# Optimization experiments

Measured on AMD Instinct MI355X. Metric: run time of the kernel, lower is better.

Reference implementation:

```python
import jax, jax.numpy as jnp
import numpy as np

N_NODES = 100000
N_EDGES = 1600000
IN_DIM = 128
HID_DIM = 64
OUT_DIM = 128
EPS = 1e-5


def setup_inputs() -> dict:
    key = jax.random.key(0)
    ks = jax.random.split(key, 10)
    feat = jax.random.normal(ks[0], (N_NODES, IN_DIM), dtype=jnp.float32)
    src = jax.random.randint(ks[1], (N_EDGES,), 0, N_NODES)
    dst = jax.random.randint(ks[2], (N_EDGES,), 0, N_NODES)
    # learned params
    gamma = jnp.ones((IN_DIM,), jnp.float32)
    beta = jnp.zeros((IN_DIM,), jnp.float32)
    Wq = jax.random.normal(ks[3], (IN_DIM, HID_DIM), jnp.float32) * 0.05
    bq = jax.random.normal(ks[4], (HID_DIM,), jnp.float32) * 0.05
    Wk = jax.random.normal(ks[5], (IN_DIM, HID_DIM), jnp.float32) * 0.05
    Wv = jax.random.normal(ks[6], (IN_DIM, OUT_DIM), jnp.float32) * 0.05
    We = jax.random.normal(ks[7], (HID_DIM, 1), jnp.float32) * 0.05
    return {"feat": feat, "src": src, "dst": dst, "gamma": gamma, "beta": beta,
            "Wq": Wq, "bq": bq, "Wk": Wk, "Wv": Wv, "We": We}


def reference(feat, src, dst, gamma, beta, Wq, bq, Wk, Wv, We):
    # BatchNorm1d (training-mode batch stats, biased variance)
    mean = jnp.mean(feat, axis=0)
    var = jnp.mean((feat - mean) ** 2, axis=0)
    x = (feat - mean) * jax.lax.rsqrt(var + EPS) * gamma + beta
    # feat_drop = 0.0 -> identity
    q = x @ Wq + bq          # [N, H]
    k = x @ Wk               # [N, H]
    v = x @ Wv               # [N, O]
    # u_add_v: src-node q + dst-node k per edge, then sigmoid and fc_e -> scalar score
    e = jax.nn.sigmoid(q[src] + k[dst]) @ We  # [E, 1]
    e = e[:, 0]                               # [E]
    # edge_softmax: softmax over incoming edges of each destination node
    m = jax.ops.segment_max(e, dst, num_segments=N_NODES)  # [N]
    ex = jnp.exp(e - m[dst])
    s = jax.ops.segment_sum(ex, dst, num_segments=N_NODES)  # [N]
    a = ex / s[dst]                                          # [E]
    # u_mul_e_sum: weighted scatter-sum of source v into destinations
    rst = jax.ops.segment_sum(v[src] * a[:, None], dst, num_segments=N_NODES)  # [N, O]
    return rst
```

## Files before the change

kernel.cpp:

```cpp
#include <hip/hip_runtime.h>
#include <math.h>

#define IN_DIM 128
#define HID 64
#define OUT_DIM 128
#define ELL_W 64
constexpr float EPS = 1e-5f;

typedef short short8 __attribute__((ext_vector_type(8)));
typedef float f32x4  __attribute__((ext_vector_type(4)));


__device__ inline ushort f2bf(float x) {
    __bf16 h = (__bf16)x;
    return *reinterpret_cast<ushort*>(&h);
}
__device__ inline short f2bfs(float x) {
    __bf16 h = (__bf16)x;
    return *reinterpret_cast<short*>(&h);
}
__device__ inline float bf2f(ushort u) {
    union { unsigned u; float f; } c; c.u = ((unsigned)u) << 16;
    return c.f;
}
__device__ inline float4 bf4_to_f4(ushort4 u) {
    return make_float4(bf2f(u.x), bf2f(u.y), bf2f(u.z), bf2f(u.w));
}

__global__ __launch_bounds__(256) void stats_kernel(
    const float* __restrict__ feat, float* __restrict__ ws, int n_nodes)
{
    int col  = threadIdx.x & 127;
    int half = threadIdx.x >> 7;
    float sum = 0.f, sq = 0.f;
    for (int r = blockIdx.x * 2 + half; r < n_nodes; r += gridDim.x * 2) {
        float x = feat[r * IN_DIM + col];
        sum += x; sq += x * x;
    }
    __shared__ float redS[256], redQ[256];
    redS[threadIdx.x] = sum; redQ[threadIdx.x] = sq;
    __syncthreads();
    if (threadIdx.x < 128) {
        sum = redS[threadIdx.x] + redS[threadIdx.x + 128];
        sq  = redQ[threadIdx.x] + redQ[threadIdx.x + 128];
        unsafeAtomicAdd(&ws[col], sum);
        unsafeAtomicAdd(&ws[128 + col], sq);
    }
}

__global__ __launch_bounds__(256) void wprep(
    const float* __restrict__ Wq, const float* __restrict__ Wk,
    const float* __restrict__ Wv, ushort* __restrict__ Bfrag)
{
    int gid  = blockIdx.x * 256 + threadIdx.x;
    int f    = gid >> 6;
    int lane = gid & 63;
    int kc = f & 3, ct = (f >> 2) & 3, w = f >> 4;
    int col   = w * 64 + ct * 16 + (lane & 15);
    int kbase = kc * 32 + (lane >> 4) * 8;
    ushort tmp[8];
    #pragma unroll
    for (int j = 0; j < 8; j++) {
        int k = kbase + j;
        float val;
        if (col < 64)       val = Wq[k * HID + col];
        else if (col < 128) val = Wk[k * HID + (col - 64)];
        else                val = Wv[k * OUT_DIM + (col - 128)];
        tmp[j] = f2bf(val);
    }
    ushort* d = &Bfrag[(f * 64 + lane) * 8];
    *(ushort4*)d       = make_ushort4(tmp[0], tmp[1], tmp[2], tmp[3]);
    *(ushort4*)(d + 4) = make_ushort4(tmp[4], tmp[5], tmp[6], tmp[7]);
}

__global__ __launch_bounds__(256) void mfma_qkv(
    const float* __restrict__ feat, const ushort* __restrict__ Bfrag,
    const float* __restrict__ bq,
    const float* __restrict__ gamma, const float* __restrict__ beta,
    const float* __restrict__ stats,
    ushort* __restrict__ qb, ushort* __restrict__ kb, ushort* __restrict__ vb,
    int n_nodes)
{
    __shared__ float sc[IN_DIM], sh[IN_DIM];
    int tid = threadIdx.x;
    if (tid < 128) {
        float inv_n = 1.0f / (float)n_nodes;
        float mean = stats[tid] * inv_n;
        float var  = stats[128 + tid] * inv_n - mean * mean;
        float s    = gamma[tid] * rsqrtf(var + EPS);
        sc[tid] = s; sh[tid] = beta[tid] - mean * s;
    }

    int w    = tid >> 6;
    int lane = tid & 63;
    int row0 = blockIdx.x * 64;
    int m    = lane & 15;
    int quad = lane >> 4;
    int nm1  = n_nodes - 1;

    short8 bfr[16];
    #pragma unroll
    for (int f = 0; f < 16; f++)
        bfr[f] = *(const short8*)&Bfrag[((w * 16 + f) * 64 + lane) * 8];

    __syncthreads();

    f32x4 acc[4][4] = {};

    #pragma unroll
    for (int kc = 0; kc < 4; kc++) {
        int koff = kc * 32 + quad * 8;
        float4 sc0 = *(const float4*)&sc[koff];
        float4 sc1 = *(const float4*)&sc[koff + 4];
        float4 sh0 = *(const float4*)&sh[koff];
        float4 sh1 = *(const float4*)&sh[koff + 4];
        short8 afr[4];
        #pragma unroll
        for (int rt = 0; rt < 4; rt++) {
            int row = row0 + rt * 16 + m;
            row = row < nm1 ? row : nm1;
            const float* fp = &feat[(size_t)row * IN_DIM + koff];
            float4 x0 = *(const float4*)fp;
            float4 x1 = *(const float4*)(fp + 4);
            afr[rt][0] = f2bfs(x0.x * sc0.x + sh0.x);
            afr[rt][1] = f2bfs(x0.y * sc0.y + sh0.y);
            afr[rt][2] = f2bfs(x0.z * sc0.z + sh0.z);
            afr[rt][3] = f2bfs(x0.w * sc0.w + sh0.w);
            afr[rt][4] = f2bfs(x1.x * sc1.x + sh1.x);
            afr[rt][5] = f2bfs(x1.y * sc1.y + sh1.y);
            afr[rt][6] = f2bfs(x1.z * sc1.z + sh1.z);
            afr[rt][7] = f2bfs(x1.w * sc1.w + sh1.w);
        }
        #pragma unroll
        for (int rt = 0; rt < 4; rt++)
            #pragma unroll
            for (int ct = 0; ct < 4; ct++)
                acc[rt][ct] = __builtin_amdgcn_mfma_f32_16x16x32_bf16(
                    afr[rt], bfr[ct * 4 + kc], acc[rt][ct], 0, 0, 0);
    }

    ushort* base; int ld, cl;
    if (w == 0)      { base = qb; ld = HID;     cl = 0; }
    else if (w == 1) { base = kb; ld = HID;     cl = 0; }
    else             { base = vb; ld = OUT_DIM; cl = (w - 2) * 64; }

    #pragma unroll
    for (int ct = 0; ct < 4; ct++) {
        int col = cl + ct * 16 + m;
        float bias = (w == 0) ? bq[ct * 16 + m] : 0.f;
        #pragma unroll
        for (int rt = 0; rt < 4; rt++) {
            int r0 = row0 + rt * 16 + quad * 4;
            #pragma unroll
            for (int r = 0; r < 4; r++)
                base[(size_t)(r0 + r) * ld + col] = f2bf(acc[rt][ct][r] + bias);
        }
    }
}

__global__ __launch_bounds__(256) void fill_ell(
    const int* __restrict__ src, const int* __restrict__ dst,
    int* __restrict__ deg, int* __restrict__ ell, int n_edges)
{
    int stride = gridDim.x * 256;
    for (int e = blockIdx.x * 256 + threadIdx.x; e < n_edges; e += stride) {
        int d = dst[e];
        int s = src[e];
        int pos = atomicAdd(&deg[d], 1);
        if (pos < ELL_W) ell[d * ELL_W + pos] = s;
    }
}

__global__ __launch_bounds__(256) void hist_kernel(
    const int* __restrict__ dst, int* __restrict__ deg, int n_edges)
{
    int e = blockIdx.x * 256 + threadIdx.x;
    if (e < n_edges) atomicAdd(&deg[dst[e]], 1);
}

#define SCAN_B 256

__global__ __launch_bounds__(256) void scan_partial(
    const int* __restrict__ deg, int* __restrict__ part, int n)
{
    int chunk = (n + SCAN_B - 1) / SCAN_B;
    int lo = blockIdx.x * chunk;
    int hi = lo + chunk; if (hi > n) hi = n;
    int s = 0;
    for (int i = lo + threadIdx.x; i < hi; i += 256) s += deg[i];
    __shared__ int red[256];
    red[threadIdx.x] = s; __syncthreads();
    for (int d = 128; d; d >>= 1) {
        if (threadIdx.x < d) red[threadIdx.x] += red[threadIdx.x + d];
        __syncthreads();
    }
    if (threadIdx.x == 0) part[blockIdx.x] = red[0];
}

__global__ __launch_bounds__(256) void scan_combine(
    int* __restrict__ part, int* __restrict__ offsets, int n)
{
    __shared__ int tmp[256];
    int t = threadIdx.x;
    int v = part[t];
    tmp[t] = v; __syncthreads();
    for (int d = 1; d < 256; d <<= 1) {
        int cur = tmp[t];
        int add = (t >= d) ? tmp[t - d] : 0;
        __syncthreads();
        tmp[t] = cur + add;
        __syncthreads();
    }
    part[t] = tmp[t] - v;
    if (t == 255) offsets[n] = tmp[255];
}

__global__ __launch_bounds__(256) void scan_final(
    const int* __restrict__ deg, const int* __restrict__ part,
    int* __restrict__ offsets, int* __restrict__ cursor, int n)
{
    __shared__ int tmp[256];
    int t = threadIdx.x;
    int chunk = (n + SCAN_B - 1) / SCAN_B;
    int lo = blockIdx.x * chunk;
    int hi = lo + chunk; if (hi > n) hi = n;
    int base = part[blockIdx.x];
    for (int i0 = lo; i0 < hi; i0 += 256) {
        int i = i0 + t;
        int d = (i < hi) ? deg[i] : 0;
        tmp[t] = d; __syncthreads();
        for (int s = 1; s < 256; s <<= 1) {
            int cur = tmp[t];
            int add = (t >= s) ? tmp[t - s] : 0;
            __syncthreads();
            tmp[t] = cur + add;
            __syncthreads();
        }
        int excl = tmp[t] - d;
        int total = tmp[255];
        if (i < hi) { offsets[i] = base + excl; cursor[i] = base + excl; }
        base += total;
        __syncthreads();
    }
}

__global__ __launch_bounds__(256) void fill_kernel(
    const int* __restrict__ src, const int* __restrict__ dst,
    int* __restrict__ cursor, int* __restrict__ csr_src, int n_edges)
{
    int e = blockIdx.x * 256 + threadIdx.x;
    if (e < n_edges) {
        int d = dst[e];
        int pos = atomicAdd(&cursor[d], 1);
        csr_src[pos] = src[e];
    }
}

__device__ inline void gather_core(
    const int* __restrict__ row, int cnt, int node, int h, int sub,
    const ushort* __restrict__ qb, const ushort* __restrict__ kb,
    const ushort* __restrict__ vb, const float* __restrict__ We,
    float* __restrict__ out)
{
    if (cnt == 0) {
        if (sub == 0) {
            float4 z = make_float4(0.f, 0.f, 0.f, 0.f);
            *(float4*)&out[node * OUT_DIM + 4 * h]      = z;
            *(float4*)&out[node * OUT_DIM + 64 + 4 * h] = z;
        }
        return;
    }

    float4 kd = bf4_to_f4(*(const ushort4*)&kb[node * HID + 4 * h]);
    float4 we = *(const float4*)&We[4 * h];

    float4 o0 = make_float4(0.f, 0.f, 0.f, 0.f);
    float4 o1 = make_float4(0.f, 0.f, 0.f, 0.f);
    float ssum = 0.f;

    for (int p0 = 0; p0 < cnt; p0 += 4) {
        int p = p0 + sub;
        bool act = (p < cnt);
        int sN = row[act ? p : 0];
        float4 qv = bf4_to_f4(*(const ushort4*)&qb[sN * HID + 4 * h]);
        float t;
        t  = we.x * __fdividef(1.f, 1.f + __expf(-(qv.x + kd.x)));
        t += we.y * __fdividef(1.f, 1.f + __expf(-(qv.y + kd.y)));
        t += we.z * __fdividef(1.f, 1.f + __expf(-(qv.z + kd.z)));
        t += we.w * __fdividef(1.f, 1.f + __expf(-(qv.w + kd.w)));
        t += __shfl_xor(t, 1);
        t += __shfl_xor(t, 2);
        t += __shfl_xor(t, 4);
        t += __shfl_xor(t, 8);
        float exv = act ? __expf(t) : 0.f;
        ssum += exv;
        float4 v0 = bf4_to_f4(*(const ushort4*)&vb[sN * OUT_DIM + 4 * h]);
        float4 v1 = bf4_to_f4(*(const ushort4*)&vb[sN * OUT_DIM + 64 + 4 * h]);
        o0.x += exv * v0.x; o0.y += exv * v0.y;
        o0.z += exv * v0.z; o0.w += exv * v0.w;
        o1.x += exv * v1.x; o1.y += exv * v1.y;
        o1.z += exv * v1.z; o1.w += exv * v1.w;
    }

    ssum += __shfl_xor(ssum, 16); ssum += __shfl_xor(ssum, 32);
    o0.x += __shfl_xor(o0.x, 16); o0.x += __shfl_xor(o0.x, 32);
    o0.y += __shfl_xor(o0.y, 16); o0.y += __shfl_xor(o0.y, 32);
    o0.z += __shfl_xor(o0.z, 16); o0.z += __shfl_xor(o0.z, 32);
    o0.w += __shfl_xor(o0.w, 16); o0.w += __shfl_xor(o0.w, 32);
    o1.x += __shfl_xor(o1.x, 16); o1.x += __shfl_xor(o1.x, 32);
    o1.y += __shfl_xor(o1.y, 16); o1.y += __shfl_xor(o1.y, 32);
    o1.z += __shfl_xor(o1.z, 16); o1.z += __shfl_xor(o1.z, 32);
    o1.w += __shfl_xor(o1.w, 16); o1.w += __shfl_xor(o1.w, 32);

    if (sub == 0) {
        float inv = (ssum > 0.f) ? __fdividef(1.f, ssum) : 0.f;
        o0.x *= inv; o0.y *= inv; o0.z *= inv; o0.w *= inv;
        o1.x *= inv; o1.y *= inv; o1.z *= inv; o1.w *= inv;
        *(float4*)&out[node * OUT_DIM + 4 * h]      = o0;
        *(float4*)&out[node * OUT_DIM + 64 + 4 * h] = o1;
    }
}

__global__ __launch_bounds__(256) void gather_ell(
    const int* __restrict__ deg, const int* __restrict__ ell,
    const ushort* __restrict__ qb, const ushort* __restrict__ kb,
    const ushort* __restrict__ vb, const float* __restrict__ We,
    float* __restrict__ out, int n_nodes)
{
    int node = (blockIdx.x * 256 + threadIdx.x) >> 6;
    int lane = threadIdx.x & 63;
    if (node >= n_nodes) return;
    int cnt = deg[node];
    cnt = cnt < ELL_W ? cnt : ELL_W;
    gather_core(&ell[(size_t)node * ELL_W], cnt, node,
                lane & 15, lane >> 4, qb, kb, vb, We, out);
}

__global__ __launch_bounds__(256) void gather_csr(
    const int* __restrict__ offsets, const int* __restrict__ csr_src,
    const ushort* __restrict__ qb, const ushort* __restrict__ kb,
    const ushort* __restrict__ vb, const float* __restrict__ We,
    float* __restrict__ out, int n_nodes)
{
    int node = (blockIdx.x * 256 + threadIdx.x) >> 6;
    int lane = threadIdx.x & 63;
    if (node >= n_nodes) return;
    int beg = offsets[node];
    int cnt = offsets[node + 1] - beg;
    gather_core(&csr_src[beg], cnt, node,
                lane & 15, lane >> 4, qb, kb, vb, We, out);
}

extern "C" void kernel_launch(void* const* d_in, const int* in_sizes, int n_in,
                              void* d_out, int out_size, void* d_ws, size_t ws_size,
                              hipStream_t stream)
{
    const float* feat  = (const float*)d_in[0];
    const int*   src   = (const int*)d_in[1];
    const int*   dst   = (const int*)d_in[2];
    const float* gamma = (const float*)d_in[3];
    const float* beta  = (const float*)d_in[4];
    const float* Wq    = (const float*)d_in[5];
    const float* bq    = (const float*)d_in[6];
    const float* Wk    = (const float*)d_in[7];
    const float* Wv    = (const float*)d_in[8];
    const float* We    = (const float*)d_in[9];

    int n_nodes = in_sizes[0] / IN_DIM;
    int n_edges = in_sizes[1];
    int n_pad   = n_nodes + 64;
    size_t bfelems = (size_t)n_pad * (HID + HID + OUT_DIM) + 64 * 64 * 8;

    float* ws = (float*)d_ws;

    size_t ell_floats = 256 + (size_t)n_nodes * (1 + ELL_W) + 4;
    size_t ell_need   = (ell_floats + (bfelems + 1) / 2) * 4;

    int eb = (n_edges + 255) / 256;

    if (ws_size >= ell_need) {
        int* deg = (int*)(ws + 256);
        int* ell = deg + n_nodes;
        size_t off = 256 + (size_t)n_nodes * (1 + ELL_W);
        off = (off + 3) & ~(size_t)3;
        ushort* qb    = (ushort*)(ws + off);
        ushort* kb    = qb + (size_t)n_pad * HID;
        ushort* vb    = kb + (size_t)n_pad * HID;
        ushort* Bfrag = vb + (size_t)n_pad * OUT_DIM;

        hipMemsetAsync(ws, 0, (256 + (size_t)n_nodes) * sizeof(float), stream);
        stats_kernel<<<256, 256, 0, stream>>>(feat, ws, n_nodes);
        wprep<<<16, 256, 0, stream>>>(Wq, Wk, Wv, Bfrag);
        fill_ell<<<(n_edges + 1023) / 1024, 256, 0, stream>>>(
            src, dst, deg, ell, n_edges);
        mfma_qkv<<<(n_nodes + 63) / 64, 256, 0, stream>>>(
            feat, Bfrag, bq, gamma, beta, ws, qb, kb, vb, n_nodes);
        long long g_threads = (long long)n_nodes * 64;
        gather_ell<<<(int)((g_threads + 255) / 256), 256, 0, stream>>>(
            deg, ell, qb, kb, vb, We, (float*)d_out, n_nodes);
    } else {
        int* deg     = (int*)(ws + 256);
        int* offsets = deg + n_nodes;
        int* cursor  = offsets + n_nodes + 1;
        int* part    = cursor + n_nodes;
        int* csr_src = part + SCAN_B;
        size_t off = 256 + 3 * (size_t)n_nodes + 1 + SCAN_B + (size_t)n_edges;
        off = (off + 3) & ~(size_t)3;
        ushort* qb    = (ushort*)(ws + off);
        ushort* kb    = qb + (size_t)n_pad * HID;
        ushort* vb    = kb + (size_t)n_pad * HID;
        ushort* Bfrag = vb + (size_t)n_pad * OUT_DIM;

        hipMemsetAsync(ws, 0, (256 + (size_t)n_nodes) * sizeof(float), stream);
        stats_kernel<<<256, 256, 0, stream>>>(feat, ws, n_nodes);
        wprep<<<16, 256, 0, stream>>>(Wq, Wk, Wv, Bfrag);
        hist_kernel<<<eb, 256, 0, stream>>>(dst, deg, n_edges);
        scan_partial<<<SCAN_B, 256, 0, stream>>>(deg, part, n_nodes);
        scan_combine<<<1, 256, 0, stream>>>(part, offsets, n_nodes);
        scan_final<<<SCAN_B, 256, 0, stream>>>(deg, part, offsets, cursor, n_nodes);
        fill_kernel<<<eb, 256, 0, stream>>>(src, dst, cursor, csr_src, n_edges);
        mfma_qkv<<<(n_nodes + 63) / 64, 256, 0, stream>>>(
            feat, Bfrag, bq, gamma, beta, ws, qb, kb, vb, n_nodes);
        long long g_threads = (long long)n_nodes * 64;
        gather_csr<<<(int)((g_threads + 255) / 256), 256, 0, stream>>>(
            offsets, csr_src, qb, kb, vb, We, (float*)d_out, n_nodes);
    }
}
```

Baseline: 421.1 us.

## Partition ELL fill by destination range across block groups with vector loads

Replaces the single-pass ELL fill with a partitioned version. Blocks are split into 8 groups, and each group handles only edges whose destination falls in its node range. The aim is to localize atomics and ELL scatter writes (which blocks, and so which L2/XCD caches, touch which nodes). Edge arrays are now read as 4-wide nontemporal vector loads. The cost is that every group re-reads the full src/dst arrays, so index traffic grows by about 8x.

```diff
diff --git a/kernel.cpp b/kernel.cpp
--- a/kernel.cpp
+++ b/kernel.cpp
@@ -5,10 +5,12 @@
 #define HID 64
 #define OUT_DIM 128
 #define ELL_W 64
+#define NPART 8
 constexpr float EPS = 1e-5f;
 
 typedef short short8 __attribute__((ext_vector_type(8)));
 typedef float f32x4  __attribute__((ext_vector_type(4)));
+typedef int   i32x4  __attribute__((ext_vector_type(4)));
 
 
 __device__ inline ushort f2bf(float x) {
@@ -158,16 +160,42 @@
     }
 }
 
-__global__ __launch_bounds__(256) void fill_ell(
+__global__ __launch_bounds__(256) void fill_ell_part(
     const int* __restrict__ src, const int* __restrict__ dst,
-    int* __restrict__ deg, int* __restrict__ ell, int n_edges)
-{
-    int stride = gridDim.x * 256;
-    for (int e = blockIdx.x * 256 + threadIdx.x; e < n_edges; e += stride) {
-        int d = dst[e];
-        int s = src[e];
-        int pos = atomicAdd(&deg[d], 1);
-        if (pos < ELL_W) ell[d * ELL_W + pos] = s;
+    int* __restrict__ deg, int* __restrict__ ell,
+    int n_edges, int part_size)
+{
+    int p  = blockIdx.x & (NPART - 1);
+    int gb = blockIdx.x >> 3;
+    int nb = gridDim.x >> 3;
+    unsigned lo = (unsigned)(p * part_size);
+    unsigned ps = (unsigned)part_size;
+
+    int idx    = gb * 256 + threadIdx.x;
+    int stride = nb * 256;
+    int n4     = n_edges >> 2;
+
+    const i32x4* dst4 = reinterpret_cast<const i32x4*>(dst);
+    const i32x4* src4 = reinterpret_cast<const i32x4*>(src);
+
+    for (int i = idx; i < n4; i += stride) {
+        i32x4 d4 = __builtin_nontemporal_load(dst4 + i);
+        i32x4 s4 = __builtin_nontemporal_load(src4 + i);
+        #pragma unroll
+        for (int j = 0; j < 4; j++) {
+            unsigned d = (unsigned)d4[j];
+            if (d - lo < ps) {
+                int pos = atomicAdd(&deg[d], 1);
+                if (pos < ELL_W) ell[(size_t)d * ELL_W + pos] = s4[j];
+            }
+        }
+    }
+    for (int e = (n4 << 2) + idx; e < n_edges; e += stride) {
+        unsigned d = (unsigned)dst[e];
+        if (d - lo < ps) {
+            int pos = atomicAdd(&deg[d], 1);
+            if (pos < ELL_W) ell[(size_t)d * ELL_W + pos] = src[e];
+        }
     }
 }
 
@@ -388,11 +416,13 @@
         ushort* vb    = kb + (size_t)n_pad * HID;
         ushort* Bfrag = vb + (size_t)n_pad * OUT_DIM;
 
+        int part_size = (n_nodes + NPART - 1) / NPART;
+
         hipMemsetAsync(ws, 0, (256 + (size_t)n_nodes) * sizeof(float), stream);
         stats_kernel<<<256, 256, 0, stream>>>(feat, ws, n_nodes);
         wprep<<<16, 256, 0, stream>>>(Wq, Wk, Wv, Bfrag);
-        fill_ell<<<(n_edges + 1023) / 1024, 256, 0, stream>>>(
-            src, dst, deg, ell, n_edges);
+        fill_ell_part<<<2048, 256, 0, stream>>>(
+            src, dst, deg, ell, n_edges, part_size);
         mfma_qkv<<<(n_nodes + 63) / 64, 256, 0, stream>>>(
             feat, Bfrag, bq, gamma, beta, ws, qb, kb, vb, n_nodes);
         long long g_threads = (long long)n_nodes * 64;
```

After: 408.8 us. -2.9%, faster.

## Replace global-atomic ELL build with binned counting sort and LDS-local ELL gather

Applied to the files above, without the earlier changes.

Drops the global atomic ELL/CSR construction. Edges are now binned by 64-node destination block through per-workgroup LDS histograms, a scan, and an LDS-atomic scatter into a packed (local dst, src) array. The gather kernel rebuilds each block's ELL in shared memory before computing. Q and V are interleaved into one 192-wide row so each source node's values are fetched together. The goal is to cut global atomic contention and the large ELL memory traffic. The cost is more kernel launches and only 64 workgroups for the hist and scatter passes, which limits parallelism. Neighbour order within a node becomes nondeterministic, and any node with more than 64 in-edges is still truncated.

```diff
diff --git a/kernel.cpp b/kernel.cpp
--- a/kernel.cpp
+++ b/kernel.cpp
@@ -5,6 +5,8 @@
 #define HID 64
 #define OUT_DIM 128
 #define ELL_W 64
+#define NWG 64
+#define SCAN_B 256
 constexpr float EPS = 1e-5f;
 
 typedef short short8 __attribute__((ext_vector_type(8)));
@@ -78,7 +80,7 @@
     const float* __restrict__ bq,
     const float* __restrict__ gamma, const float* __restrict__ beta,
     const float* __restrict__ stats,
-    ushort* __restrict__ qb, ushort* __restrict__ kb, ushort* __restrict__ vb,
+    ushort* __restrict__ qvb, ushort* __restrict__ kb,
     int n_nodes)
 {
     __shared__ float sc[IN_DIM], sh[IN_DIM];
@@ -140,9 +142,8 @@
     }
 
     ushort* base; int ld, cl;
-    if (w == 0)      { base = qb; ld = HID;     cl = 0; }
-    else if (w == 1) { base = kb; ld = HID;     cl = 0; }
-    else             { base = vb; ld = OUT_DIM; cl = (w - 2) * 64; }
+    if (w == 1)      { base = kb;  ld = HID; cl = 0; }
+    else             { base = qvb; ld = 192; cl = (w == 0) ? 0 : 64 * (w - 1); }
 
     #pragma unroll
     for (int ct = 0; ct < 4; ct++) {
@@ -158,27 +159,22 @@
     }
 }
 
-__global__ __launch_bounds__(256) void fill_ell(
-    const int* __restrict__ src, const int* __restrict__ dst,
-    int* __restrict__ deg, int* __restrict__ ell, int n_edges)
-{
-    int stride = gridDim.x * 256;
-    for (int e = blockIdx.x * 256 + threadIdx.x; e < n_edges; e += stride) {
-        int d = dst[e];
-        int s = src[e];
-        int pos = atomicAdd(&deg[d], 1);
-        if (pos < ELL_W) ell[d * ELL_W + pos] = s;
-    }
-}
-
-__global__ __launch_bounds__(256) void hist_kernel(
-    const int* __restrict__ dst, int* __restrict__ deg, int n_edges)
-{
-    int e = blockIdx.x * 256 + threadIdx.x;
-    if (e < n_edges) atomicAdd(&deg[dst[e]], 1);
-}
-
-#define SCAN_B 256
+__global__ __launch_bounds__(256) void hist_bins(
+    const int* __restrict__ dst, int* __restrict__ histT,
+    int n_edges, int nbk, int chunk)
+{
+    extern __shared__ int cnt[];
+    int w = blockIdx.x, t = threadIdx.x;
+    for (int b = t; b < nbk; b += 256) cnt[b] = 0;
+    __syncthreads();
+    int lo = w * chunk;
+    int hi = lo + chunk; if (hi > n_edges) hi = n_edges;
+    for (int e = lo + t; e < hi; e += 256)
+        atomicAdd(&cnt[dst[e] >> 6], 1);
+    __syncthreads();
+    for (int b = t; b < nbk; b += 256)
+        histT[b * NWG + w] = cnt[b];
+}
 
 __global__ __launch_bounds__(256) void scan_partial(
     const int* __restrict__ deg, int* __restrict__ part, int n)
@@ -244,23 +240,29 @@
     }
 }
 
-__global__ __launch_bounds__(256) void fill_kernel(
+__global__ __launch_bounds__(256) void scatter_bins(
     const int* __restrict__ src, const int* __restrict__ dst,
-    int* __restrict__ cursor, int* __restrict__ csr_src, int n_edges)
-{
-    int e = blockIdx.x * 256 + threadIdx.x;
-    if (e < n_edges) {
+    const int* __restrict__ offs, int* __restrict__ packed,
+    int n_edges, int nbk, int chunk)
+{
+    extern __shared__ int cur[];
+    int w = blockIdx.x, t = threadIdx.x;
+    for (int b = t; b < nbk; b += 256) cur[b] = offs[b * NWG + w];
+    __syncthreads();
+    int lo = w * chunk;
+    int hi = lo + chunk; if (hi > n_edges) hi = n_edges;
+    for (int e = lo + t; e < hi; e += 256) {
         int d = dst[e];
-        int pos = atomicAdd(&cursor[d], 1);
-        csr_src[pos] = src[e];
-    }
-}
-
-__device__ inline void gather_core(
-    const int* __restrict__ row, int cnt, int node, int h, int sub,
-    const ushort* __restrict__ qb, const ushort* __restrict__ kb,
-    const ushort* __restrict__ vb, const float* __restrict__ We,
-    float* __restrict__ out)
+        int b = d >> 6;
+        int pos = atomicAdd(&cur[b], 1);
+        packed[pos] = (int)(((unsigned)(d & 63) << 26) | (unsigned)src[e]);
+    }
+}
+
+__device__ __forceinline__ void gather_core(
+    const int* row, int cnt, int node, int h, int sub,
+    const ushort* __restrict__ qvb, const ushort* __restrict__ kb,
+    const float* __restrict__ We, float* __restrict__ out)
 {
     if (cnt == 0) {
         if (sub == 0) {
@@ -282,20 +284,21 @@
         int p = p0 + sub;
         bool act = (p < cnt);
         int sN = row[act ? p : 0];
-        float4 qv = bf4_to_f4(*(const ushort4*)&qb[sN * HID + 4 * h]);
+        const ushort* qv = qvb + (size_t)sN * 192;
+        float4 qq = bf4_to_f4(*(const ushort4*)(qv + 4 * h));
         float t;
-        t  = we.x * __fdividef(1.f, 1.f + __expf(-(qv.x + kd.x)));
-        t += we.y * __fdividef(1.f, 1.f + __expf(-(qv.y + kd.y)));
-        t += we.z * __fdividef(1.f, 1.f + __expf(-(qv.z + kd.z)));
-        t += we.w * __fdividef(1.f, 1.f + __expf(-(qv.w + kd.w)));
+        t  = we.x * __fdividef(1.f, 1.f + __expf(-(qq.x + kd.x)));
+        t += we.y * __fdividef(1.f, 1.f + __expf(-(qq.y + kd.y)));
+        t += we.z * __fdividef(1.f, 1.f + __expf(-(qq.z + kd.z)));
+        t += we.w * __fdividef(1.f, 1.f + __expf(-(qq.w + kd.w)));
         t += __shfl_xor(t, 1);
         t += __shfl_xor(t, 2);
         t += __shfl_xor(t, 4);
         t += __shfl_xor(t, 8);
         float exv = act ? __expf(t) : 0.f;
         ssum += exv;
-        float4 v0 = bf4_to_f4(*(const ushort4*)&vb[sN * OUT_DIM + 4 * h]);
-        float4 v1 = bf4_to_f4(*(const ushort4*)&vb[sN * OUT_DIM + 64 + 4 * h]);
+        float4 v0 = bf4_to_f4(*(const ushort4*)(qv + 64 + 4 * h));
+        float4 v1 = bf4_to_f4(*(const ushort4*)(qv + 128 + 4 * h));
         o0.x += exv * v0.x; o0.y += exv * v0.y;
         o0.z += exv * v0.z; o0.w += exv * v0.w;
         o1.x += exv * v1.x; o1.y += exv * v1.y;
@@ -321,34 +324,42 @@
     }
 }
 
-__global__ __launch_bounds__(256) void gather_ell(
-    const int* __restrict__ deg, const int* __restrict__ ell,
-    const ushort* __restrict__ qb, const ushort* __restrict__ kb,
-    const ushort* __restrict__ vb, const float* __restrict__ We,
+__global__ __launch_bounds__(256) void gather_fused(
+    const int* __restrict__ offs, const int* __restrict__ packed,
+    const ushort* __restrict__ qvb, const ushort* __restrict__ kb,
+    const float* __restrict__ We,
     float* __restrict__ out, int n_nodes)
 {
-    int node = (blockIdx.x * 256 + threadIdx.x) >> 6;
-    int lane = threadIdx.x & 63;
-    if (node >= n_nodes) return;
-    int cnt = deg[node];
-    cnt = cnt < ELL_W ? cnt : ELL_W;
-    gather_core(&ell[(size_t)node * ELL_W], cnt, node,
-                lane & 15, lane >> 4, qb, kb, vb, We, out);
-}
-
-__global__ __launch_bounds__(256) void gather_csr(
-    const int* __restrict__ offsets, const int* __restrict__ csr_src,
-    const ushort* __restrict__ qb, const ushort* __restrict__ kb,
-    const ushort* __restrict__ vb, const float* __restrict__ We,
-    float* __restrict__ out, int n_nodes)
-{
-    int node = (blockIdx.x * 256 + threadIdx.x) >> 6;
-    int lane = threadIdx.x & 63;
-    if (node >= n_nodes) return;
-    int beg = offsets[node];
-    int cnt = offsets[node + 1] - beg;
-    gather_core(&csr_src[beg], cnt, node,
-                lane & 15, lane >> 4, qb, kb, vb, We, out);
+    __shared__ int deg_l[64];
+    __shared__ int ell_l[64][ELL_W];
+    int b = blockIdx.x;
+    int t = threadIdx.x;
+    if (t < 64) deg_l[t] = 0;
+    __syncthreads();
+
+    int beg = offs[b * NWG];
+    int end = offs[(b + 1) * NWG];
+    for (int e = beg + t; e < end; e += 256) {
+        int p = packed[e];
+        int dl = (int)((unsigned)p >> 26);
+        int pos = atomicAdd(&deg_l[dl], 1);
+        if (pos < ELL_W) ell_l[dl][pos] = p & 0x03FFFFFF;
+    }
+    __syncthreads();
+
+    int wv   = t >> 6;
+    int lane = t & 63;
+    int h    = lane & 15;
+    int sub  = lane >> 4;
+    #pragma unroll 1
+    for (int i = 0; i < 16; i++) {
+        int dl = wv * 16 + i;
+        int node = (b << 6) + dl;
+        if (node >= n_nodes) break;
+        int cnt = deg_l[dl];
+        cnt = cnt < ELL_W ? cnt : ELL_W;
+        gather_core(&ell_l[dl][0], cnt, node, h, sub, qvb, kb, We, out);
+    }
 }
 
 extern "C" void kernel_launch(void* const* d_in, const int* in_sizes, int n_in,
@@ -369,60 +380,37 @@
     int n_nodes = in_sizes[0] / IN_DIM;
     int n_edges = in_sizes[1];
     int n_pad   = n_nodes + 64;
-    size_t bfelems = (size_t)n_pad * (HID + HID + OUT_DIM) + 64 * 64 * 8;
+    int nbk     = (n_nodes + 63) >> 6;
+    int nidx    = nbk * NWG;
+    int chunk   = (n_edges + NWG - 1) / NWG;
 
     float* ws = (float*)d_ws;
 
-    size_t ell_floats = 256 + (size_t)n_nodes * (1 + ELL_W) + 4;
-    size_t ell_need   = (ell_floats + (bfelems + 1) / 2) * 4;
-
-    int eb = (n_edges + 255) / 256;
-
-    if (ws_size >= ell_need) {
-        int* deg = (int*)(ws + 256);
-        int* ell = deg + n_nodes;
-        size_t off = 256 + (size_t)n_nodes * (1 + ELL_W);
-        off = (off + 3) & ~(size_t)3;
-        ushort* qb    = (ushort*)(ws + off);
-        ushort* kb    = qb + (size_t)n_pad * HID;
-        ushort* vb    = kb + (size_t)n_pad * HID;
-        ushort* Bfrag = vb + (size_t)n_pad * OUT_DIM;
-
-        hipMemsetAsync(ws, 0, (256 + (size_t)n_nodes) * sizeof(float), stream);
-        stats_kernel<<<256, 256, 0, stream>>>(feat, ws, n_nodes);
-        wprep<<<16, 256, 0, stream>>>(Wq, Wk, Wv, Bfrag);
-        fill_ell<<<(n_edges + 1023) / 1024, 256, 0, stream>>>(
-            src, dst, deg, ell, n_edges);
-        mfma_qkv<<<(n_nodes + 63) / 64, 256, 0, stream>>>(
-            feat, Bfrag, bq, gamma, beta, ws, qb, kb, vb, n_nodes);
-        long long g_threads = (long long)n_nodes * 64;
-        gather_ell<<<(int)((g_threads + 255) / 256), 256, 0, stream>>>(
-            deg, ell, qb, kb, vb, We, (float*)d_out, n_nodes);
-    } else {
-        int* deg     = (int*)(ws + 256);
-        int* offsets = deg + n_nodes;
-        int* cursor  = offsets + n_nodes + 1;
-        int* part    = cursor + n_nodes;
-        int* csr_src = part + SCAN_B;
-        size_t off = 256 + 3 * (size_t)n_nodes + 1 + SCAN_B + (size_t)n_edges;
-        off = (off + 3) & ~(size_t)3;
-        ushort* qb    = (ushort*)(ws + off);
-        ushort* kb    = qb + (size_t)n_pad * HID;
-        ushort* vb    = kb + (size_t)n_pad * HID;
-        ushort* Bfrag = vb + (size_t)n_pad * OUT_DIM;
-
-        hipMemsetAsync(ws, 0, (256 + (size_t)n_nodes) * sizeof(float), stream);
-        stats_kernel<<<256, 256, 0, stream>>>(feat, ws, n_nodes);
-        wprep<<<16, 256, 0, stream>>>(Wq, Wk, Wv, Bfrag);
-        hist_kernel<<<eb, 256, 0, stream>>>(dst, deg, n_edges);
-        scan_partial<<<SCAN_B, 256, 0, stream>>>(deg, part, n_nodes);
-        scan_combine<<<1, 256, 0, stream>>>(part, offsets, n_nodes);
-        scan_final<<<SCAN_B, 256, 0, stream>>>(deg, part, offsets, cursor, n_nodes);
-        fill_kernel<<<eb, 256, 0, stream>>>(src, dst, cursor, csr_src, n_edges);
-        mfma_qkv<<<(n_nodes + 63) / 64, 256, 0, stream>>>(
-            feat, Bfrag, bq, gamma, beta, ws, qb, kb, vb, n_nodes);
-        long long g_threads = (long long)n_nodes * 64;
-        gather_csr<<<(int)((g_threads + 255) / 256), 256, 0, stream>>>(
-            offsets, csr_src, qb, kb, vb, We, (float*)d_out, n_nodes);
-    }
-}
+    int* histT  = (int*)(ws + 256);
+    int* offs   = histT + nidx;
+    int* part   = offs + nidx + 1;
+    int* cursor = part + SCAN_B;
+    int* packed = cursor + nidx + 1;
+    size_t off = 256 + (size_t)(nidx) + (nidx + 1) + SCAN_B + (nidx + 1)
+               + (size_t)n_edges;
+    off = (off + 3) & ~(size_t)3;
+    ushort* qvb   = (ushort*)(ws + off);
+    ushort* kb    = qvb + (size_t)n_pad * 192;
+    ushort* Bfrag = kb + (size_t)n_pad * HID;
+
+    size_t lds_bins = (size_t)nbk * sizeof(int);
+
+    hipMemsetAsync(ws, 0, 256 * sizeof(float), stream);
+    stats_kernel<<<256, 256, 0, stream>>>(feat, ws, n_nodes);
+    wprep<<<16, 256, 0, stream>>>(Wq, Wk, Wv, Bfrag);
+    hist_bins<<<NWG, 256, lds_bins, stream>>>(dst, histT, n_edges, nbk, chunk);
+    scan_partial<<<SCAN_B, 256, 0, stream>>>(histT, part, nidx);
+    scan_combine<<<1, 256, 0, stream>>>(part, offs, nidx);
+    scan_final<<<SCAN_B, 256, 0, stream>>>(histT, part, offs, cursor, nidx);
+    scatter_bins<<<NWG, 256, lds_bins, stream>>>(
+        src, dst, offs, packed, n_edges, nbk, chunk);
+    mfma_qkv<<<(n_nodes + 63) / 64, 256, 0, stream>>>(
+        feat, Bfrag, bq, gamma, beta, ws, qvb, kb, n_nodes);
+    gather_fused<<<nbk, 256, 0, stream>>>(
+        offs, packed, qvb, kb, We, (float*)d_out, n_nodes);
+}
```

Measured after the change: 488.9 us. 16.1% more time.
